# Kernel tuning notes

Hardware: AMD Instinct MI355X
Metric: run time of the kernel (lower is better)

Reference implementation:

```python
import jax, jax.numpy as jnp
import numpy as np

VOCAB = 32000
D_MODEL = 1024


def setup_inputs() -> dict:
    key = jax.random.key(0)
    k = jax.random.split(key, 8)
    B, H, T, S = 8, 16, 128, 512
    src = jax.random.randint(k[0], (B, S), 0, VOCAB)
    decode_output = jax.random.normal(k[1], (B, T, D_MODEL), dtype=jnp.float32)
    decode_attn = jax.random.uniform(k[2], (B, H, T, S), dtype=jnp.float32)
    memory = jax.random.normal(k[3], (B, S, D_MODEL), dtype=jnp.float32)
    W_gen = jax.random.normal(k[4], (VOCAB, D_MODEL), dtype=jnp.float32) * (1.0 / np.sqrt(D_MODEL))
    b_gen = jnp.zeros((VOCAB,), dtype=jnp.float32)
    W_prob = jax.random.normal(k[5], (1, 2 * D_MODEL), dtype=jnp.float32) * (1.0 / np.sqrt(2 * D_MODEL))
    b_prob = jnp.zeros((1,), dtype=jnp.float32)
    return {"src": src, "decode_output": decode_output, "decode_attn": decode_attn,
            "memory": memory, "W_gen": W_gen, "b_gen": b_gen,
            "W_prob": W_prob, "b_prob": b_prob}


def reference(src, decode_output, decode_attn, memory, W_gen, b_gen, W_prob, b_prob):
    # mean over heads: [B, T, S]
    attn = jnp.mean(decode_attn, axis=1)
    B, T, S = attn.shape
    V = W_gen.shape[0]

    # generation logits: [B, T, V]
    gen_logits = jnp.einsum('btd,vd->btv', decode_output, W_gen) + b_gen

    # context vector: [B, T, D]
    context = jnp.einsum('bts,bsd->btd', attn, memory)

    # scatter-add copy distribution over vocab: [B, T, V]
    src_exp = jnp.broadcast_to(src[:, None, :], (B, T, S))  # token ids per step
    b_idx = jnp.arange(B)[:, None, None]
    t_idx = jnp.arange(T)[None, :, None]
    copy_logits = jnp.zeros((B, T, V), dtype=attn.dtype).at[b_idx, t_idx, src_exp].add(attn)

    # copy gate: sigmoid(Linear([context; decode_output])) -> [B, T, 1]
    cat = jnp.concatenate([context, decode_output], axis=-1)
    prob = jax.nn.sigmoid(jnp.einsum('btd,od->bto', cat, W_prob) + b_prob)

    gen_p = prob * jax.nn.softmax(gen_logits, axis=-1)
    copy_p = (1.0 - prob) * jax.nn.softmax(copy_logits, axis=-1)
    final = gen_p + copy_p
    return jnp.log(final).reshape(-1, V)
```

## Files before the change

### kernel.cpp

```cpp
#include <hip/hip_runtime.h>
#include <hip/hip_bf16.h>
#include <cstddef>
#include <cstdint>

#define BB 8
#define HH 16
#define TT 128
#define SS 512
#define DD 1024
#define VV 32000
#define MM (BB * TT)

typedef float f32x4 __attribute__((ext_vector_type(4)));
typedef short short8v __attribute__((ext_vector_type(8)));
typedef unsigned short ushort8v __attribute__((ext_vector_type(8)));

__device__ __forceinline__ unsigned short f2bf(float x) {
    __hip_bfloat16 h = __float2bfloat16(x);
    return __builtin_bit_cast(unsigned short, h);
}
__device__ __forceinline__ float bf2f(unsigned short u) {
    unsigned int x = ((unsigned int)u) << 16;
    return __builtin_bit_cast(float, x);
}

__device__ __forceinline__ float wave_sum(float v) {
#pragma unroll
    for (int o = 1; o < 64; o <<= 1) v += __shfl_xor(v, o);
    return v;
}
__device__ __forceinline__ float wave_max(float v) {
#pragma unroll
    for (int o = 1; o < 64; o <<= 1) v = fmaxf(v, __shfl_xor(v, o));
    return v;
}
__device__ __forceinline__ float block_sum(float v, float* red, int tid) {
    v = wave_sum(v);
    __syncthreads();
    if ((tid & 63) == 0) red[tid >> 6] = v;
    __syncthreads();
    return red[0] + red[1] + red[2] + red[3];
}
__device__ __forceinline__ float block_max(float v, float* red, int tid) {
    v = wave_max(v);
    __syncthreads();
    if ((tid & 63) == 0) red[tid >> 6] = v;
    __syncthreads();
    return fmaxf(fmaxf(red[0], red[1]), fmaxf(red[2], red[3]));
}

__global__ void k_pm_init(int* pos_map, float* zg) {
    int i = blockIdx.x * 256 + threadIdx.x;
    if (i < BB * VV) pos_map[i] = 0x7fffffff;
    if (i < MM) zg[i] = 0.0f;
}

__global__ void k_pm_build(const int* __restrict__ src, int* pos_map) {
    int b = blockIdx.x, s = threadIdx.x;
    int tok = src[b * SS + s];
    atomicMin(&pos_map[b * VV + tok], s);
}

__global__ __launch_bounds__(256) void k_cast(const float* __restrict__ in,
                                              unsigned short* __restrict__ outp, int n8) {
    int stride = gridDim.x * 256;
    for (int i = blockIdx.x * 256 + threadIdx.x; i < n8; i += stride) {
        const float4* p = reinterpret_cast<const float4*>(in + (size_t)i * 8);
        float4 a = p[0], b = p[1];
        ushort8v u;
        u[0] = f2bf(a.x); u[1] = f2bf(a.y); u[2] = f2bf(a.z); u[3] = f2bf(a.w);
        u[4] = f2bf(b.x); u[5] = f2bf(b.y); u[6] = f2bf(b.z); u[7] = f2bf(b.w);
        *reinterpret_cast<ushort8v*>(outp + (size_t)i * 8) = u;
    }
}

__global__ __launch_bounds__(256) void k_vecdots(const float* __restrict__ memory,
                                                 const float* __restrict__ dec,
                                                 const float* __restrict__ wprob,
                                                 float* mw, float* dw) {
    int row = blockIdx.x * 4 + (threadIdx.x >> 6);
    int lane = threadIdx.x & 63;
    const float4* srcv;
    const float4* wv;
    if (row < BB * SS) {
        srcv = reinterpret_cast<const float4*>(memory + (size_t)row * DD);
        wv = reinterpret_cast<const float4*>(wprob);
    } else {
        srcv = reinterpret_cast<const float4*>(dec + (size_t)(row - BB * SS) * DD);
        wv = reinterpret_cast<const float4*>(wprob + DD);
    }
    float sum = 0.f;
#pragma unroll
    for (int k = 0; k < 4; ++k) {
        int idx = lane + 64 * k;
        float4 a = srcv[idx];
        float4 w = wv[idx];
        sum += a.x * w.x + a.y * w.y + a.z * w.z + a.w * w.w;
    }
    sum = wave_sum(sum);
    if (lane == 0) {
        if (row < BB * SS) mw[row] = sum;
        else dw[row - BB * SS] = sum;
    }
}

__global__ __launch_bounds__(256) void k_row(const float* __restrict__ dattn,
                                             const int* __restrict__ src,
                                             const int* __restrict__ pos_map,
                                             const float* __restrict__ mw,
                                             const float* __restrict__ dw,
                                             const float* __restrict__ bprob,
                                             float* __restrict__ e_vals,
                                             float* __restrict__ prob,
                                             float* __restrict__ zc,
                                             float* __restrict__ c0) {
    int bt = blockIdx.x;
    int b = bt >> 7;
    int t = bt & 127;
    int tid = threadIdx.x;
    __shared__ float a_row[SS];
    __shared__ float vals[SS];
    __shared__ float red[4];

    for (int s = tid; s < SS; s += 256) {
        const float* base = dattn + ((size_t)b * HH * TT + t) * SS + s;
        float sum = 0.f;
#pragma unroll
        for (int h = 0; h < HH; ++h) sum += base[(size_t)h * TT * SS];
        a_row[s] = sum * 0.0625f;
        vals[s] = 0.f;
    }
    __syncthreads();
    for (int s = tid; s < SS; s += 256) {
        int rep = pos_map[b * VV + src[b * SS + s]];
        atomicAdd(&vals[rep], a_row[s]);
    }
    __syncthreads();
    float psum = 0.f;
    for (int s = tid; s < SS; s += 256) psum += a_row[s] * mw[b * SS + s];
    psum = block_sum(psum, red, tid);
    float z = psum + dw[bt] + bprob[0];
    float p = 1.0f / (1.0f + __expf(-z));
    float mxv = -3.4e38f;
    for (int s = tid; s < SS; s += 256) {
        int rep = pos_map[b * VV + src[b * SS + s]];
        if (rep == s) mxv = fmaxf(mxv, vals[s]);
    }
    mxv = block_max(mxv, red, tid);
    float m_c = fmaxf(0.0f, mxv);
    float sexp = 0.f, cnt = 0.f;
    for (int s = tid; s < SS; s += 256) {
        int rep = pos_map[b * VV + src[b * SS + s]];
        float e = 0.0f;
        if (rep == s) {
            e = __expf(vals[s] - m_c);
            sexp += e;
            cnt += 1.0f;
        }
        e_vals[(size_t)bt * SS + s] = e;
    }
    sexp = block_sum(sexp, red, tid);
    cnt = block_sum(cnt, red, tid);
    if (tid == 0) {
        prob[bt] = p;
        zc[bt] = ((float)VV - cnt) * __expf(-m_c) + sexp;
        c0[bt] = __expf(-m_c);
    }
}

#define Bk 64
#define NKT 16

#define AS1 __attribute__((address_space(1)))
#define AS3 __attribute__((address_space(3)))

template <int EPI>
__global__ __launch_bounds__(512, 4) void k_gemm_bf(const unsigned short* __restrict__ Abf,
                                                    const unsigned short* __restrict__ Wbf,
                                                    const float* __restrict__ bgen,
                                                    float* __restrict__ out,
                                                    unsigned short* __restrict__ ebuf,
                                                    float* __restrict__ zg) {
    __shared__ unsigned short lds[24576];

    int tid = threadIdx.x;
    int p = blockIdx.x;
    int wg = (p & 7) * 125 + (p >> 3);
    int mt = wg & 7, nt = wg >> 3;
    int m0 = mt * 128, v0 = nt * 256;

    int lane = tid & 63, w = tid >> 6;
    int wm = w & 1, wn = w >> 1;

    int srow = tid >> 3;
    int schunk = (tid & 7) ^ (srow & 7);
    const unsigned short* gA = Abf + (size_t)(m0 + srow) * DD + schunk * 8;
    const unsigned short* gB = Wbf + (size_t)(v0 + srow) * DD + schunk * 8;

#define STAGE(T) do {                                                                  \
    size_t ko_ = (size_t)(T) * Bk;                                                     \
    _Pragma("unroll")                                                                  \
    for (int q = 0; q < 2; ++q)                                                        \
        __builtin_amdgcn_global_load_lds(                                              \
            (const AS1 void*)(gA + (size_t)q * 64 * DD + ko_),                         \
            (AS3 void*)(lds + q * 4096 + tid * 8), 16, 0, 0);                          \
    _Pragma("unroll")                                                                  \
    for (int q = 0; q < 4; ++q)                                                        \
        __builtin_amdgcn_global_load_lds(                                              \
            (const AS1 void*)(gB + (size_t)q * 64 * DD + ko_),                         \
            (AS3 void*)(lds + 8192 + q * 4096 + tid * 8), 16, 0, 0);                   \
} while (0)

    int lr = lane & 15, kg = lane >> 4, l7s = (lane & 15) & 7;

    f32x4 acc[4][4] = {};

    STAGE(0);
    asm volatile("s_waitcnt vmcnt(0)" ::: "memory");
    __builtin_amdgcn_s_barrier();

    for (int t = 0; t < NKT; ++t) {
        short8v af[4], bfr[4];
        {
            const int c = (kg ^ l7s) * 8;
#pragma unroll
            for (int i = 0; i < 4; ++i)
                af[i] = *reinterpret_cast<const short8v*>(&lds[(wm * 64 + i * 16 + lr) * 64 + c]);
#pragma unroll
            for (int j = 0; j < 4; ++j)
                bfr[j] = *reinterpret_cast<const short8v*>(&lds[8192 + (wn * 64 + j * 16 + lr) * 64 + c]);
            asm volatile("s_waitcnt lgkmcnt(0)" ::: "memory");
            __builtin_amdgcn_sched_barrier(0);
            __builtin_amdgcn_s_setprio(1);
#pragma unroll
            for (int i = 0; i < 4; ++i)
#pragma unroll
                for (int j = 0; j < 4; ++j)
                    acc[i][j] = __builtin_amdgcn_mfma_f32_16x16x32_bf16(af[i], bfr[j], acc[i][j], 0, 0, 0);
            __builtin_amdgcn_s_setprio(0);
        }
        {
            const int c = ((4 + kg) ^ l7s) * 8;
#pragma unroll
            for (int i = 0; i < 4; ++i)
                af[i] = *reinterpret_cast<const short8v*>(&lds[(wm * 64 + i * 16 + lr) * 64 + c]);
#pragma unroll
            for (int j = 0; j < 4; ++j)
                bfr[j] = *reinterpret_cast<const short8v*>(&lds[8192 + (wn * 64 + j * 16 + lr) * 64 + c]);
            asm volatile("s_waitcnt lgkmcnt(0)" ::: "memory");
            __builtin_amdgcn_sched_barrier(0);
            __builtin_amdgcn_s_barrier();
            if (t + 1 < NKT) STAGE(t + 1);
            __builtin_amdgcn_s_setprio(1);
#pragma unroll
            for (int i = 0; i < 4; ++i)
#pragma unroll
                for (int j = 0; j < 4; ++j)
                    acc[i][j] = __builtin_amdgcn_mfma_f32_16x16x32_bf16(af[i], bfr[j], acc[i][j], 0, 0, 0);
            __builtin_amdgcn_s_setprio(0);
            if (t + 1 < NKT) {
                asm volatile("s_waitcnt vmcnt(0)" ::: "memory");
                __builtin_amdgcn_s_barrier();
            }
        }
    }
#undef STAGE

    int colb = lane & 15, rgrp = lane >> 4;
#pragma unroll
    for (int i = 0; i < 4; ++i) {
        float es0 = 0.f, es1 = 0.f, es2 = 0.f, es3 = 0.f;
        int gmb = m0 + wm * 64 + i * 16 + rgrp * 4;
#pragma unroll
        for (int j = 0; j < 4; ++j) {
            int gv = v0 + wn * 64 + j * 16 + colb;
            float bgj = bgen[gv];
            float v0f = acc[i][j][0] + bgj;
            float v1f = acc[i][j][1] + bgj;
            float v2f = acc[i][j][2] + bgj;
            float v3f = acc[i][j][3] + bgj;
            float e0 = __expf(v0f), e1 = __expf(v1f), e2 = __expf(v2f), e3 = __expf(v3f);
            if constexpr (EPI == 1) {
                ebuf[(size_t)(gmb + 0) * VV + gv] = f2bf(e0);
                ebuf[(size_t)(gmb + 1) * VV + gv] = f2bf(e1);
                ebuf[(size_t)(gmb + 2) * VV + gv] = f2bf(e2);
                ebuf[(size_t)(gmb + 3) * VV + gv] = f2bf(e3);
            } else {
                out[(size_t)(gmb + 0) * VV + gv] = v0f;
                out[(size_t)(gmb + 1) * VV + gv] = v1f;
                out[(size_t)(gmb + 2) * VV + gv] = v2f;
                out[(size_t)(gmb + 3) * VV + gv] = v3f;
            }
            es0 += e0; es1 += e1; es2 += e2; es3 += e3;
        }
        float es[4] = {es0, es1, es2, es3};
#pragma unroll
        for (int rr = 0; rr < 4; ++rr) {
            float e = es[rr];
            e += __shfl_xor(e, 1); e += __shfl_xor(e, 2);
            e += __shfl_xor(e, 4); e += __shfl_xor(e, 8);
            if (colb == 0) atomicAdd(&zg[gmb + rr], e);
        }
    }
}

#define FBb 128
#define FLDK 40

__global__ __launch_bounds__(256) void k_gemm_f32(const float* __restrict__ A,
                                                  const float* __restrict__ Wg,
                                                  const float* __restrict__ bgen,
                                                  float* __restrict__ out,
                                                  float* __restrict__ zg) {
    __shared__ unsigned short As[FBb * FLDK];
    __shared__ unsigned short Bs[FBb * FLDK];
    int tid = threadIdx.x;
    int bid = blockIdx.x;
    int mt = bid & 7;
    int nt = bid >> 3;
    int m0 = mt * FBb, v0 = nt * FBb;
    int lane = tid & 63, wid = tid >> 6;
    int wr = (wid >> 1) * 64, wc = (wid & 1) * 64;
    int lr = lane & 15, lk = (lane >> 4) << 3;
    int r = tid >> 1, c0 = (tid & 1) << 4;

    f32x4 acc[4][4] = {};

    for (int k0 = 0; k0 < DD; k0 += 32) {
        {
            const float4* pa = reinterpret_cast<const float4*>(A + (size_t)(m0 + r) * DD + k0 + c0);
            float4 x0 = pa[0], x1 = pa[1], x2 = pa[2], x3 = pa[3];
            ushort8v u0, u1;
            u0[0] = f2bf(x0.x); u0[1] = f2bf(x0.y); u0[2] = f2bf(x0.z); u0[3] = f2bf(x0.w);
            u0[4] = f2bf(x1.x); u0[5] = f2bf(x1.y); u0[6] = f2bf(x1.z); u0[7] = f2bf(x1.w);
            u1[0] = f2bf(x2.x); u1[1] = f2bf(x2.y); u1[2] = f2bf(x2.z); u1[3] = f2bf(x2.w);
            u1[4] = f2bf(x3.x); u1[5] = f2bf(x3.y); u1[6] = f2bf(x3.z); u1[7] = f2bf(x3.w);
            *reinterpret_cast<ushort8v*>(&As[r * FLDK + c0]) = u0;
            *reinterpret_cast<ushort8v*>(&As[r * FLDK + c0 + 8]) = u1;

            const float4* pb = reinterpret_cast<const float4*>(Wg + (size_t)(v0 + r) * DD + k0 + c0);
            float4 y0 = pb[0], y1 = pb[1], y2 = pb[2], y3 = pb[3];
            ushort8v w0, w1;
            w0[0] = f2bf(y0.x); w0[1] = f2bf(y0.y); w0[2] = f2bf(y0.z); w0[3] = f2bf(y0.w);
            w0[4] = f2bf(y1.x); w0[5] = f2bf(y1.y); w0[6] = f2bf(y1.z); w0[7] = f2bf(y1.w);
            w1[0] = f2bf(y2.x); w1[1] = f2bf(y2.y); w1[2] = f2bf(y2.z); w1[3] = f2bf(y2.w);
            w1[4] = f2bf(y3.x); w1[5] = f2bf(y3.y); w1[6] = f2bf(y3.z); w1[7] = f2bf(y3.w);
            *reinterpret_cast<ushort8v*>(&Bs[r * FLDK + c0]) = w0;
            *reinterpret_cast<ushort8v*>(&Bs[r * FLDK + c0 + 8]) = w1;
        }
        __syncthreads();

        short8v af[4], bfr[4];
#pragma unroll
        for (int i = 0; i < 4; ++i)
            af[i] = *reinterpret_cast<const short8v*>(&As[(wr + i * 16 + lr) * FLDK + lk]);
#pragma unroll
        for (int j = 0; j < 4; ++j)
            bfr[j] = *reinterpret_cast<const short8v*>(&Bs[(wc + j * 16 + lr) * FLDK + lk]);
#pragma unroll
        for (int i = 0; i < 4; ++i)
#pragma unroll
            for (int j = 0; j < 4; ++j)
                acc[i][j] = __builtin_amdgcn_mfma_f32_16x16x32_bf16(af[i], bfr[j], acc[i][j], 0, 0, 0);
        __syncthreads();
    }

    int colb = lane & 15;
    int rgrp = lane >> 4;
#pragma unroll
    for (int i = 0; i < 4; ++i) {
        float es0 = 0.f, es1 = 0.f, es2 = 0.f, es3 = 0.f;
        int gmb = m0 + wr + i * 16 + rgrp * 4;
#pragma unroll
        for (int j = 0; j < 4; ++j) {
            int gv = v0 + wc + j * 16 + colb;
            float bgj = bgen[gv];
            float v0f = acc[i][j][0] + bgj;
            float v1f = acc[i][j][1] + bgj;
            float v2f = acc[i][j][2] + bgj;
            float v3f = acc[i][j][3] + bgj;
            out[(size_t)(gmb + 0) * VV + gv] = v0f;
            out[(size_t)(gmb + 1) * VV + gv] = v1f;
            out[(size_t)(gmb + 2) * VV + gv] = v2f;
            out[(size_t)(gmb + 3) * VV + gv] = v3f;
            es0 += __expf(v0f); es1 += __expf(v1f);
            es2 += __expf(v2f); es3 += __expf(v3f);
        }
        float es[4] = {es0, es1, es2, es3};
#pragma unroll
        for (int rr = 0; rr < 4; ++rr) {
            float e = es[rr];
            e += __shfl_xor(e, 1); e += __shfl_xor(e, 2);
            e += __shfl_xor(e, 4); e += __shfl_xor(e, 8);
            if (colb == 0) atomicAdd(&zg[gmb + rr], e);
        }
    }
}

template <int RD16>
__global__ __launch_bounds__(256) void k_final(float* __restrict__ gen,
                                               const unsigned short* __restrict__ ebuf,
                                               const int* __restrict__ pos_map,
                                               const float* __restrict__ e_vals,
                                               const float* __restrict__ prob,
                                               const float* __restrict__ zc,
                                               const float* __restrict__ c0,
                                               const float* __restrict__ zg) {
    int m = blockIdx.x;
    int b = m >> 7;
    int tid = threadIdx.x;
    float p = prob[m];
    float A1 = p / zg[m];
    float A2 = (1.0f - p) / zc[m];
    float cc = c0[m];
    const float* ev = e_vals + (size_t)m * SS;
    float4* row = reinterpret_cast<float4*>(gen + (size_t)m * VV);
    const int4* pm = reinterpret_cast<const int4*>(pos_map + b * VV);
    if constexpr (RD16 == 1) {
        const ushort8v* erow = reinterpret_cast<const ushort8v*>(ebuf + (size_t)m * VV);
        for (int i = tid; i < VV / 8; i += 256) {
            ushort8v ee = erow[i];
            int4 rp0 = pm[2 * i], rp1 = pm[2 * i + 1];
            float4 o0, o1;
            o0.x = __logf(A1 * bf2f(ee[0]) + A2 * ((rp0.x < SS) ? ev[rp0.x] : cc));
            o0.y = __logf(A1 * bf2f(ee[1]) + A2 * ((rp0.y < SS) ? ev[rp0.y] : cc));
            o0.z = __logf(A1 * bf2f(ee[2]) + A2 * ((rp0.z < SS) ? ev[rp0.z] : cc));
            o0.w = __logf(A1 * bf2f(ee[3]) + A2 * ((rp0.w < SS) ? ev[rp0.w] : cc));
            o1.x = __logf(A1 * bf2f(ee[4]) + A2 * ((rp1.x < SS) ? ev[rp1.x] : cc));
            o1.y = __logf(A1 * bf2f(ee[5]) + A2 * ((rp1.y < SS) ? ev[rp1.y] : cc));
            o1.z = __logf(A1 * bf2f(ee[6]) + A2 * ((rp1.z < SS) ? ev[rp1.z] : cc));
            o1.w = __logf(A1 * bf2f(ee[7]) + A2 * ((rp1.w < SS) ? ev[rp1.w] : cc));
            row[2 * i] = o0;
            row[2 * i + 1] = o1;
        }
    } else {
        for (int i = tid; i < VV / 4; i += 256) {
            float4 g = row[i];
            int4 rp = pm[i];
            float4 o;
            o.x = __logf(A1 * __expf(g.x) + A2 * ((rp.x < SS) ? ev[rp.x] : cc));
            o.y = __logf(A1 * __expf(g.y) + A2 * ((rp.y < SS) ? ev[rp.y] : cc));
            o.z = __logf(A1 * __expf(g.z) + A2 * ((rp.z < SS) ? ev[rp.z] : cc));
            o.w = __logf(A1 * __expf(g.w) + A2 * ((rp.w < SS) ? ev[rp.w] : cc));
            row[i] = o;
        }
    }
}

extern "C" void kernel_launch(void* const* d_in, const int* in_sizes, int n_in,
                              void* d_out, int out_size, void* d_ws, size_t ws_size,
                              hipStream_t stream) {
    const int* src = (const int*)d_in[0];
    const float* dec = (const float*)d_in[1];
    const float* dattn = (const float*)d_in[2];
    const float* mem = (const float*)d_in[3];
    const float* wgen = (const float*)d_in[4];
    const float* bgen = (const float*)d_in[5];
    const float* wprob = (const float*)d_in[6];
    const float* bprob = (const float*)d_in[7];
    float* out = (float*)d_out;
    char* ws = (char*)d_ws;

    int* pos_map = (int*)(ws + 0);
    float* e_vals = (float*)(ws + 1048576);
    float* mw   = (float*)(ws + 3145728);
    float* dw   = (float*)(ws + 3145728 + 16384);
    float* prob = (float*)(ws + 3145728 + 20480);
    float* zc   = (float*)(ws + 3145728 + 24576);
    float* c0   = (float*)(ws + 3145728 + 28672);
    float* zg   = (float*)(ws + 3145728 + 32768);
    unsigned short* Wbf = (unsigned short*)(ws + 3211264);
    unsigned short* Abf = (unsigned short*)(ws + 3211264 + 65536000);
    unsigned short* Ebf = (unsigned short*)(ws + 3211264 + 65536000 + 2097152);
    const size_t NEEDED  = 3211264ull + 65536000ull + 2097152ull;
    const size_t NEEDED2 = NEEDED + 65536000ull;

    k_pm_init<<<(BB * VV + 255) / 256, 256, 0, stream>>>(pos_map, zg);
    k_pm_build<<<BB, SS, 0, stream>>>(src, pos_map);
    k_vecdots<<<(BB * SS + MM) / 4, 256, 0, stream>>>(mem, dec, wprob, mw, dw);
    k_row<<<MM, 256, 0, stream>>>(dattn, src, pos_map, mw, dw, bprob, e_vals, prob, zc, c0);

    if (ws_size >= NEEDED) {
        k_cast<<<2048, 256, 0, stream>>>(wgen, Wbf, VV * DD / 8);
        k_cast<<<512, 256, 0, stream>>>(dec, Abf, MM * DD / 8);
        if (ws_size >= NEEDED2) {
            k_gemm_bf<1><<<(MM / 128) * (VV / 256), 512, 0, stream>>>(Abf, Wbf, bgen, out, Ebf, zg);
            k_final<1><<<MM, 256, 0, stream>>>(out, Ebf, pos_map, e_vals, prob, zc, c0, zg);
        } else {
            k_gemm_bf<0><<<(MM / 128) * (VV / 256), 512, 0, stream>>>(Abf, Wbf, bgen, out, Ebf, zg);
            k_final<0><<<MM, 256, 0, stream>>>(out, Ebf, pos_map, e_vals, prob, zc, c0, zg);
        }
    } else {
        k_gemm_f32<<<(MM / FBb) * (VV / FBb), 256, 0, stream>>>(dec, wgen, bgen, out, zg);
        k_final<0><<<MM, 256, 0, stream>>>(out, Ebf, pos_map, e_vals, prob, zc, c0, zg);
    }
}
```

Before: 230.1 us.

## Triple-buffer GEMM k-loop with 32-wide K tiles and two-ahead prefetch

Reworks the bf16 generation GEMM main loop from a double-pass 64-wide K tile with a single buffer to a triple-buffered ring of 32-wide K tiles. Each tile is prefetched two iterations ahead, and each iteration now has only one barrier. The aim is to hide global-to-LDS latency behind MFMA work and cut synchronisation. In exchange, LDS use per block rises, which may lower resident blocks per CU, and the XOR swizzle on LDS rows is dropped, which may add bank conflicts on the fragment reads.

```diff
diff --git a/kernel.cpp b/kernel.cpp
--- a/kernel.cpp
+++ b/kernel.cpp
@@ -168,8 +168,8 @@
     }
 }
 
-#define Bk 64
-#define NKT 16
+#define NKT 32
+#define BUFE 12288
 
 #define AS1 __attribute__((address_space(1)))
 #define AS3 __attribute__((address_space(3)))
@@ -181,7 +181,7 @@
                                                     float* __restrict__ out,
                                                     unsigned short* __restrict__ ebuf,
                                                     float* __restrict__ zg) {
-    __shared__ unsigned short lds[24576];
+    __shared__ unsigned short lds[3 * BUFE];
 
     int tid = threadIdx.x;
     int p = blockIdx.x;
@@ -192,78 +192,65 @@
     int lane = tid & 63, w = tid >> 6;
     int wm = w & 1, wn = w >> 1;
 
-    int srow = tid >> 3;
-    int schunk = (tid & 7) ^ (srow & 7);
-    const unsigned short* gA = Abf + (size_t)(m0 + srow) * DD + schunk * 8;
-    const unsigned short* gB = Wbf + (size_t)(v0 + srow) * DD + schunk * 8;
-
-#define STAGE(T) do {                                                                  \
-    size_t ko_ = (size_t)(T) * Bk;                                                     \
+    int srow = tid >> 2;
+    int scol = (tid & 3) << 3;
+    const unsigned short* gA = Abf + (size_t)(m0 + srow) * DD + scol;
+    const unsigned short* gB = Wbf + (size_t)(v0 + srow) * DD + scol;
+
+#define STAGE(T, BI) do {                                                              \
+    size_t ko_ = (size_t)(T) * 32;                                                     \
+    __builtin_amdgcn_global_load_lds(                                                  \
+        (const AS1 void*)(gA + ko_),                                                   \
+        (AS3 void*)(lds + (BI) * BUFE + tid * 8), 16, 0, 0);                           \
+    __builtin_amdgcn_global_load_lds(                                                  \
+        (const AS1 void*)(gB + ko_),                                                   \
+        (AS3 void*)(lds + (BI) * BUFE + 4096 + tid * 8), 16, 0, 0);                    \
+    __builtin_amdgcn_global_load_lds(                                                  \
+        (const AS1 void*)(gB + (size_t)128 * DD + ko_),                                \
+        (AS3 void*)(lds + (BI) * BUFE + 8192 + tid * 8), 16, 0, 0);                    \
+} while (0)
+
+    int lr = lane & 15, kg8 = (lane >> 4) << 3;
+    const unsigned short* arow = lds + (wm * 64 + lr) * 32 + kg8;
+    const unsigned short* brow = lds + 4096 + (wn * 64 + lr) * 32 + kg8;
+
+    f32x4 acc[4][4] = {};
+
+#define ITER(T, BI, DO_STAGE, VM)  do {                                                \
+    __builtin_amdgcn_s_barrier();                                                      \
+    short8v af[4], bfr[4];                                                             \
     _Pragma("unroll")                                                                  \
-    for (int q = 0; q < 2; ++q)                                                        \
-        __builtin_amdgcn_global_load_lds(                                              \
-            (const AS1 void*)(gA + (size_t)q * 64 * DD + ko_),                         \
-            (AS3 void*)(lds + q * 4096 + tid * 8), 16, 0, 0);                          \
+    for (int i = 0; i < 4; ++i)                                                        \
+        af[i] = *reinterpret_cast<const short8v*>(arow + (BI) * BUFE + i * (16 * 32)); \
     _Pragma("unroll")                                                                  \
-    for (int q = 0; q < 4; ++q)                                                        \
-        __builtin_amdgcn_global_load_lds(                                              \
-            (const AS1 void*)(gB + (size_t)q * 64 * DD + ko_),                         \
-            (AS3 void*)(lds + 8192 + q * 4096 + tid * 8), 16, 0, 0);                   \
+    for (int j = 0; j < 4; ++j)                                                        \
+        bfr[j] = *reinterpret_cast<const short8v*>(brow + (BI) * BUFE + j * (16 * 32));\
+    if (DO_STAGE) STAGE((T) + 2, ((BI) + 2) % 3);                                      \
+    asm volatile("s_waitcnt lgkmcnt(0)" ::: "memory");                                 \
+    __builtin_amdgcn_sched_barrier(0);                                                 \
+    __builtin_amdgcn_s_setprio(1);                                                     \
+    _Pragma("unroll")                                                                  \
+    for (int i = 0; i < 4; ++i)                                                        \
+        _Pragma("unroll")                                                              \
+        for (int j = 0; j < 4; ++j)                                                    \
+            acc[i][j] = __builtin_amdgcn_mfma_f32_16x16x32_bf16(af[i], bfr[j], acc[i][j], 0, 0, 0); \
+    __builtin_amdgcn_s_setprio(0);                                                     \
+    if ((VM) == 3) asm volatile("s_waitcnt vmcnt(3)" ::: "memory");                    \
+    else if ((VM) == 0) asm volatile("s_waitcnt vmcnt(0)" ::: "memory");               \
 } while (0)
 
-    int lr = lane & 15, kg = lane >> 4, l7s = (lane & 15) & 7;
-
-    f32x4 acc[4][4] = {};
-
-    STAGE(0);
-    asm volatile("s_waitcnt vmcnt(0)" ::: "memory");
-    __builtin_amdgcn_s_barrier();
-
-    for (int t = 0; t < NKT; ++t) {
-        short8v af[4], bfr[4];
-        {
-            const int c = (kg ^ l7s) * 8;
-#pragma unroll
-            for (int i = 0; i < 4; ++i)
-                af[i] = *reinterpret_cast<const short8v*>(&lds[(wm * 64 + i * 16 + lr) * 64 + c]);
-#pragma unroll
-            for (int j = 0; j < 4; ++j)
-                bfr[j] = *reinterpret_cast<const short8v*>(&lds[8192 + (wn * 64 + j * 16 + lr) * 64 + c]);
-            asm volatile("s_waitcnt lgkmcnt(0)" ::: "memory");
-            __builtin_amdgcn_sched_barrier(0);
-            __builtin_amdgcn_s_setprio(1);
-#pragma unroll
-            for (int i = 0; i < 4; ++i)
-#pragma unroll
-                for (int j = 0; j < 4; ++j)
-                    acc[i][j] = __builtin_amdgcn_mfma_f32_16x16x32_bf16(af[i], bfr[j], acc[i][j], 0, 0, 0);
-            __builtin_amdgcn_s_setprio(0);
-        }
-        {
-            const int c = ((4 + kg) ^ l7s) * 8;
-#pragma unroll
-            for (int i = 0; i < 4; ++i)
-                af[i] = *reinterpret_cast<const short8v*>(&lds[(wm * 64 + i * 16 + lr) * 64 + c]);
-#pragma unroll
-            for (int j = 0; j < 4; ++j)
-                bfr[j] = *reinterpret_cast<const short8v*>(&lds[8192 + (wn * 64 + j * 16 + lr) * 64 + c]);
-            asm volatile("s_waitcnt lgkmcnt(0)" ::: "memory");
-            __builtin_amdgcn_sched_barrier(0);
-            __builtin_amdgcn_s_barrier();
-            if (t + 1 < NKT) STAGE(t + 1);
-            __builtin_amdgcn_s_setprio(1);
-#pragma unroll
-            for (int i = 0; i < 4; ++i)
-#pragma unroll
-                for (int j = 0; j < 4; ++j)
-                    acc[i][j] = __builtin_amdgcn_mfma_f32_16x16x32_bf16(af[i], bfr[j], acc[i][j], 0, 0, 0);
-            __builtin_amdgcn_s_setprio(0);
-            if (t + 1 < NKT) {
-                asm volatile("s_waitcnt vmcnt(0)" ::: "memory");
-                __builtin_amdgcn_s_barrier();
-            }
-        }
-    }
+    STAGE(0, 0);
+    STAGE(1, 1);
+    asm volatile("s_waitcnt vmcnt(3)" ::: "memory");
+
+    for (int t = 0; t < NKT - 2; t += 3) {
+        ITER(t + 0, 0, true, 3);
+        ITER(t + 1, 1, true, 3);
+        ITER(t + 2, 2, true, 3);
+    }
+    ITER(30, 0, false, 0);
+    ITER(31, 1, false, -1);
+#undef ITER
 #undef STAGE
 
     int colb = lane & 15, rgrp = lane >> 4;
```

Result: faster. 222.9 us, median of 3 (-3.2%).
